# Performance work log

Hardware: AMD Instinct MI355X
Metric: run time of the kernel (lower is better)

Reference implementation:

```python
import jax, jax.numpy as jnp
import numpy as np

B, S, H = 64, 2048, 768
LAM = 0.0  # sparsegen-lin lambda (lam=0 -> sparsemax)
NEG = -1e30


def setup_inputs() -> dict:
    key = jax.random.key(0)
    k1, k2, k3, k4, k5 = jax.random.split(key, 5)
    hidden = jax.random.normal(k1, (B, S, H), jnp.float32)
    # contiguous entity spans of random length (>=16 valid tokens per example)
    lengths = jax.random.randint(k2, (B,), 16, S)
    mask1d = (jnp.arange(S)[None, :] < lengths[:, None]).astype(jnp.float32)
    token_mask = jnp.broadcast_to(mask1d[:, :, None], (B, S, H))
    pooled_tokens = jax.random.normal(k3, (B, H), jnp.float32)
    w_align = jax.random.normal(k4, (2 * H,), jnp.float32) * 0.02
    b_align = jax.random.normal(k5, (1,), jnp.float32) * 0.02
    return {"hidden": hidden, "token_mask": token_mask,
            "pooled_tokens": pooled_tokens, "w_align": w_align, "b_align": b_align}


def sparsegen_masked(scores, valid, lam):
    """Batched sparsegen-lin over valid positions only.
    scores: [B, S] float, valid: [B, S] bool. Returns probs [B, S] (0 at invalid).
    Matches per-example torch SparsegenLin applied to masked_select'd scores.
    """
    n = scores.shape[-1]
    zmax = jnp.max(jnp.where(valid, scores, -jnp.inf), axis=-1, keepdims=True)
    z = scores - zmax                                # subtract max over valid
    z_sortable = jnp.where(valid, z, NEG)
    zs = -jnp.sort(-z_sortable, axis=-1)             # descending; valid first
    n_valid = jnp.sum(valid, axis=-1, keepdims=True)
    ks = jnp.arange(1, n + 1, dtype=scores.dtype)[None, :]
    sorted_valid = ks <= n_valid.astype(scores.dtype)
    zs_m = jnp.where(sorted_valid, zs, 0.0)
    csum = jnp.cumsum(zs_m, axis=-1)
    bound = 1.0 - lam + ks * zs_m
    is_gt = (bound > csum) & sorted_valid
    k = jnp.maximum(jnp.max(jnp.where(is_gt, ks, 0.0), axis=-1, keepdims=True), 1.0)
    tau = (jnp.sum(jnp.where(is_gt, zs_m, 0.0), axis=-1, keepdims=True) - 1.0 + lam) / k
    ps = jnp.maximum((z - tau) / (1.0 - lam), 0.0)
    return jnp.where(valid, ps, 0.0)


def reference(hidden, token_mask, pooled_tokens, w_align, b_align):
    masked_hidden = hidden * token_mask                       # [B,S,H]
    tokens_rep_masked = pooled_tokens[:, None, :] * token_mask  # [B,S,H]
    # alignment_model(cat(tokens_rep_masked, masked_hidden)) -> [B,S]
    scores = (jnp.einsum('bsh,h->bs', tokens_rep_masked, w_align[:H])
              + jnp.einsum('bsh,h->bs', masked_hidden, w_align[H:])
              + b_align[0])
    attn_mask = token_mask[:, :, 0] > 0                       # [B,S] bool
    attention_probs = sparsegen_masked(scores, attn_mask, LAM)[:, :, None]  # [B,S,1]
    pooled = jnp.sum(masked_hidden * attention_probs, axis=1)  # [B,H]
    # insize == outsize -> output_layer is skipped (projected = pooled)
    return pooled, attention_probs
```

## Files before the change

kernel.cpp:

```cpp
#include <hip/hip_runtime.h>
#include <hip/hip_bf16.h>
#include <cstdint>
#include <cstddef>

#define BB 64
#define SS 2048
#define HH 768
#define LAM 0.0f
#define NEGV -1e30f

__global__ void scores_kernel(const float* __restrict__ hidden,
                              const float* __restrict__ token_mask,
                              const float* __restrict__ w_align,
                              float* __restrict__ scores) {
    int row = blockIdx.x * 4 + (threadIdx.x >> 6);
    int lane = threadIdx.x & 63;
    float m = token_mask[(size_t)row * HH];
    if (m == 0.0f) {
        if (lane == 0) scores[row] = NEGV;
        return;
    }
    const float* hrow = hidden + (size_t)row * HH;
    const float* w2 = w_align + HH;
    float acc = 0.f;
#pragma unroll
    for (int r = 0; r < 3; ++r) {
        int idx = r * 256 + lane * 4;
        float4 h = *reinterpret_cast<const float4*>(hrow + idx);
        float4 w = *reinterpret_cast<const float4*>(w2 + idx);
        acc += h.x * w.x + h.y * w.y + h.z * w.z + h.w * w.w;
    }
#pragma unroll
    for (int off = 32; off >= 1; off >>= 1) acc += __shfl_xor(acc, off);
    if (lane == 0) scores[row] = acc;
}

__device__ inline float breduce_sum(float v, float* red, int t) {
#pragma unroll
    for (int off = 32; off >= 1; off >>= 1) v += __shfl_xor(v, off);
    if ((t & 63) == 0) red[t >> 6] = v;
    __syncthreads();
    if (t < 16) {
        float x = red[t];
#pragma unroll
        for (int off = 8; off >= 1; off >>= 1) x += __shfl_xor(x, off);
        if (t == 0) red[0] = x;
    }
    __syncthreads();
    float r = red[0];
    __syncthreads();
    return r;
}

__device__ inline float breduce_max(float v, float* red, int t) {
#pragma unroll
    for (int off = 32; off >= 1; off >>= 1) v = fmaxf(v, __shfl_xor(v, off));
    if ((t & 63) == 0) red[t >> 6] = v;
    __syncthreads();
    if (t < 16) {
        float x = red[t];
#pragma unroll
        for (int off = 8; off >= 1; off >>= 1) x = fmaxf(x, __shfl_xor(x, off));
        if (t == 0) red[0] = x;
    }
    __syncthreads();
    float r = red[0];
    __syncthreads();
    return r;
}

__device__ inline float2 breduce_sum2(float a, float c, float2* red2, int t) {
#pragma unroll
    for (int off = 32; off >= 1; off >>= 1) {
        a += __shfl_xor(a, off);
        c += __shfl_xor(c, off);
    }
    if ((t & 63) == 0) red2[t >> 6] = make_float2(a, c);
    __syncthreads();
    if (t < 16) {
        float2 x = red2[t];
#pragma unroll
        for (int off = 8; off >= 1; off >>= 1) {
            x.x += __shfl_xor(x.x, off);
            x.y += __shfl_xor(x.y, off);
        }
        if (t == 0) red2[0] = x;
    }
    __syncthreads();
    float2 r = red2[0];
    __syncthreads();
    return r;
}

__global__ __launch_bounds__(1024, 1) void sparsemax_pool_kernel(
        const float* __restrict__ hidden,
        const float* __restrict__ pooled_tokens,
        const float* __restrict__ w_align,
        const float* __restrict__ b_align,
        const float* __restrict__ scores,
        float* __restrict__ out) {
    __shared__ float pl[SS];
    __shared__ int   sidx[SS];
    __shared__ float spv[SS];
    __shared__ float red[32];
    __shared__ float2 red2[16];
    __shared__ int   icnt;

    const int b = blockIdx.x;
    const int t = threadIdx.x;
    const int i0 = t, i1 = t + 1024;

    float v = (t < HH) ? pooled_tokens[b * HH + t] * w_align[t] : 0.f;
    float dotP = breduce_sum(v, red, t) + b_align[0];

    float r0 = scores[b * SS + i0];
    float r1 = scores[b * SS + i1];
    bool valid0 = r0 > -1e29f;
    bool valid1 = r1 > -1e29f;
    float s0 = r0 + dotP;
    float s1 = r1 + dotP;

    float mx = fmaxf(valid0 ? s0 : -INFINITY, valid1 ? s1 : -INFINITY);
    float zmax = breduce_max(mx, red, t);

    float z0 = valid0 ? (s0 - zmax) : NEGV;
    float z1 = valid1 ? (s1 - zmax) : NEGV;

    float tau = -1.0f;
#pragma unroll 1
    for (int it = 0; it < 50; ++it) {
        float a = (z0 > tau ? z0 : 0.f) + (z1 > tau ? z1 : 0.f);
        float c = (z0 > tau ? 1.f : 0.f) + (z1 > tau ? 1.f : 0.f);
        float2 sc = breduce_sum2(a, c, red2, t);
        float tn = (sc.x - 1.f + LAM) / sc.y;
        if (tn == tau) break;
        tau = tn;
    }

    const float inv = 1.f / (1.f - LAM);
    float p0 = valid0 ? fmaxf((z0 - tau) * inv, 0.f) : 0.f;
    float p1 = valid1 ? fmaxf((z1 - tau) * inv, 0.f) : 0.f;
    pl[i0] = p0;
    pl[i1] = p1;
    out[BB * HH + b * SS + i0] = p0;
    out[BB * HH + b * SS + i1] = p1;
    __syncthreads();

    if (t < 64) {
        int cnt = 0;
        for (int base = 0; base < SS; base += 64) {
            float p = pl[base + t];
            unsigned long long bal = __ballot(p > 0.f);
            if (p > 0.f) {
                int pos = cnt + (int)__popcll(bal & ((1ull << t) - 1ull));
                sidx[pos] = base + t;
                spv[pos] = p;
            }
            cnt += (int)__popcll(bal);
        }
        if (t == 0) icnt = cnt;
    }
    __syncthreads();
    int cnt = icnt;

    if (t < HH) {
        float acc = 0.f;
        for (int j = 0; j < cnt; ++j) {
            acc += spv[j] * hidden[(size_t)(b * SS + sidx[j]) * HH + t];
        }
        out[b * HH + t] = acc;
    }
}

extern "C" void kernel_launch(void* const* d_in, const int* in_sizes, int n_in,
                              void* d_out, int out_size, void* d_ws, size_t ws_size,
                              hipStream_t stream) {
    const float* hidden        = (const float*)d_in[0];
    const float* token_mask    = (const float*)d_in[1];
    const float* pooled_tokens = (const float*)d_in[2];
    const float* b_align       = (const float*)d_in[4];
    const float* w_align       = (const float*)d_in[3];
    float* out = (float*)d_out;

    float* scores_ws;
    if (ws_size >= (size_t)BB * SS * sizeof(float)) {
        scores_ws = (float*)d_ws;
    } else {
        scores_ws = out + BB * HH;
    }

    scores_kernel<<<dim3((BB * SS) / 4), dim3(256), 0, stream>>>(
        hidden, token_mask, w_align, scores_ws);

    sparsemax_pool_kernel<<<dim3(BB), dim3(1024), 0, stream>>>(
        hidden, pooled_tokens, w_align, b_align, scores_ws, out);
}
```

Baseline: 51.25 us.

## Assign one wavefront per batch row for sparsemax threshold and pooling

```diff
diff --git a/kernel.cpp b/kernel.cpp
--- a/kernel.cpp
+++ b/kernel.cpp
@@ -35,141 +35,104 @@
     if (lane == 0) scores[row] = acc;
 }
 
-__device__ inline float breduce_sum(float v, float* red, int t) {
-#pragma unroll
-    for (int off = 32; off >= 1; off >>= 1) v += __shfl_xor(v, off);
-    if ((t & 63) == 0) red[t >> 6] = v;
-    __syncthreads();
-    if (t < 16) {
-        float x = red[t];
-#pragma unroll
-        for (int off = 8; off >= 1; off >>= 1) x += __shfl_xor(x, off);
-        if (t == 0) red[0] = x;
-    }
-    __syncthreads();
-    float r = red[0];
-    __syncthreads();
-    return r;
-}
-
-__device__ inline float breduce_max(float v, float* red, int t) {
-#pragma unroll
-    for (int off = 32; off >= 1; off >>= 1) v = fmaxf(v, __shfl_xor(v, off));
-    if ((t & 63) == 0) red[t >> 6] = v;
-    __syncthreads();
-    if (t < 16) {
-        float x = red[t];
-#pragma unroll
-        for (int off = 8; off >= 1; off >>= 1) x = fmaxf(x, __shfl_xor(x, off));
-        if (t == 0) red[0] = x;
-    }
-    __syncthreads();
-    float r = red[0];
-    __syncthreads();
-    return r;
-}
-
-__device__ inline float2 breduce_sum2(float a, float c, float2* red2, int t) {
-#pragma unroll
-    for (int off = 32; off >= 1; off >>= 1) {
-        a += __shfl_xor(a, off);
-        c += __shfl_xor(c, off);
-    }
-    if ((t & 63) == 0) red2[t >> 6] = make_float2(a, c);
-    __syncthreads();
-    if (t < 16) {
-        float2 x = red2[t];
-#pragma unroll
-        for (int off = 8; off >= 1; off >>= 1) {
-            x.x += __shfl_xor(x.x, off);
-            x.y += __shfl_xor(x.y, off);
-        }
-        if (t == 0) red2[0] = x;
-    }
-    __syncthreads();
-    float2 r = red2[0];
-    __syncthreads();
-    return r;
-}
-
-__global__ __launch_bounds__(1024, 1) void sparsemax_pool_kernel(
+__global__ __launch_bounds__(256, 1) void tau_pool_kernel(
         const float* __restrict__ hidden,
         const float* __restrict__ pooled_tokens,
         const float* __restrict__ w_align,
         const float* __restrict__ b_align,
         const float* __restrict__ scores,
         float* __restrict__ out) {
-    __shared__ float pl[SS];
-    __shared__ int   sidx[SS];
-    __shared__ float spv[SS];
-    __shared__ float red[32];
-    __shared__ float2 red2[16];
-    __shared__ int   icnt;
+    const int b = (blockIdx.x * 256 + threadIdx.x) >> 6;
+    const int lane = threadIdx.x & 63;
 
-    const int b = blockIdx.x;
-    const int t = threadIdx.x;
-    const int i0 = t, i1 = t + 1024;
+    const float* pt = pooled_tokens + b * HH;
+    float dp = 0.f;
+#pragma unroll
+    for (int i = 0; i < 3; ++i) {
+        int idx = i * 256 + lane * 4;
+        float4 a = *reinterpret_cast<const float4*>(pt + idx);
+        float4 w = *reinterpret_cast<const float4*>(w_align + idx);
+        dp += a.x * w.x + a.y * w.y + a.z * w.z + a.w * w.w;
+    }
+#pragma unroll
+    for (int off = 32; off >= 1; off >>= 1) dp += __shfl_xor(dp, off);
+    dp += b_align[0];
 
-    float v = (t < HH) ? pooled_tokens[b * HH + t] * w_align[t] : 0.f;
-    float dotP = breduce_sum(v, red, t) + b_align[0];
+    const float* sc = scores + b * SS;
+    float z[32];
+#pragma unroll
+    for (int i = 0; i < 8; ++i) {
+        float4 v = *reinterpret_cast<const float4*>(sc + i * 256 + lane * 4);
+        z[i * 4 + 0] = v.x + dp;
+        z[i * 4 + 1] = v.y + dp;
+        z[i * 4 + 2] = v.z + dp;
+        z[i * 4 + 3] = v.w + dp;
+    }
 
-    float r0 = scores[b * SS + i0];
-    float r1 = scores[b * SS + i1];
-    bool valid0 = r0 > -1e29f;
-    bool valid1 = r1 > -1e29f;
-    float s0 = r0 + dotP;
-    float s1 = r1 + dotP;
-
-    float mx = fmaxf(valid0 ? s0 : -INFINITY, valid1 ? s1 : -INFINITY);
-    float zmax = breduce_max(mx, red, t);
-
-    float z0 = valid0 ? (s0 - zmax) : NEGV;
-    float z1 = valid1 ? (s1 - zmax) : NEGV;
+    float mx = z[0];
+#pragma unroll
+    for (int i = 1; i < 32; ++i) mx = fmaxf(mx, z[i]);
+#pragma unroll
+    for (int off = 32; off >= 1; off >>= 1) mx = fmaxf(mx, __shfl_xor(mx, off));
+#pragma unroll
+    for (int i = 0; i < 32; ++i) z[i] -= mx;
 
     float tau = -1.0f;
 #pragma unroll 1
     for (int it = 0; it < 50; ++it) {
-        float a = (z0 > tau ? z0 : 0.f) + (z1 > tau ? z1 : 0.f);
-        float c = (z0 > tau ? 1.f : 0.f) + (z1 > tau ? 1.f : 0.f);
-        float2 sc = breduce_sum2(a, c, red2, t);
-        float tn = (sc.x - 1.f + LAM) / sc.y;
+        float a = 0.f, c = 0.f;
+#pragma unroll
+        for (int i = 0; i < 32; ++i) {
+            bool g = z[i] > tau;
+            a += g ? z[i] : 0.f;
+            c += g ? 1.f : 0.f;
+        }
+#pragma unroll
+        for (int off = 32; off >= 1; off >>= 1) {
+            a += __shfl_xor(a, off);
+            c += __shfl_xor(c, off);
+        }
+        float tn = (a - 1.f + LAM) / c;
         if (tn == tau) break;
         tau = tn;
     }
 
     const float inv = 1.f / (1.f - LAM);
-    float p0 = valid0 ? fmaxf((z0 - tau) * inv, 0.f) : 0.f;
-    float p1 = valid1 ? fmaxf((z1 - tau) * inv, 0.f) : 0.f;
-    pl[i0] = p0;
-    pl[i1] = p1;
-    out[BB * HH + b * SS + i0] = p0;
-    out[BB * HH + b * SS + i1] = p1;
-    __syncthreads();
+    float p[32];
+#pragma unroll
+    for (int i = 0; i < 32; ++i) p[i] = fmaxf((z[i] - tau) * inv, 0.f);
+    float* po = out + BB * HH + b * SS;
+#pragma unroll
+    for (int i = 0; i < 8; ++i) {
+        float4 v = make_float4(p[i * 4 + 0], p[i * 4 + 1], p[i * 4 + 2], p[i * 4 + 3]);
+        *reinterpret_cast<float4*>(po + i * 256 + lane * 4) = v;
+    }
 
-    if (t < 64) {
-        int cnt = 0;
-        for (int base = 0; base < SS; base += 64) {
-            float p = pl[base + t];
-            unsigned long long bal = __ballot(p > 0.f);
-            if (p > 0.f) {
-                int pos = cnt + (int)__popcll(bal & ((1ull << t) - 1ull));
-                sidx[pos] = base + t;
-                spv[pos] = p;
+    float acc[12];
+#pragma unroll
+    for (int j = 0; j < 12; ++j) acc[j] = 0.f;
+    const float* hb = hidden + (size_t)b * SS * HH;
+#pragma unroll 1
+    for (int i = 0; i < 8; ++i) {
+#pragma unroll 1
+        for (int c = 0; c < 4; ++c) {
+            float pv = p[i * 4 + c];
+            unsigned long long m = __ballot(pv > 0.f);
+            while (m) {
+                int src = __ffsll((long long)m) - 1;
+                m &= m - 1;
+                float pb = __shfl(pv, src);
+                int sidx = i * 256 + src * 4 + c;
+                const float* hrow = hb + (size_t)sidx * HH;
+#pragma unroll
+                for (int j = 0; j < 12; ++j)
+                    acc[j] += pb * hrow[j * 64 + lane];
             }
-            cnt += (int)__popcll(bal);
         }
-        if (t == 0) icnt = cnt;
     }
-    __syncthreads();
-    int cnt = icnt;
-
-    if (t < HH) {
-        float acc = 0.f;
-        for (int j = 0; j < cnt; ++j) {
-            acc += spv[j] * hidden[(size_t)(b * SS + sidx[j]) * HH + t];
-        }
-        out[b * HH + t] = acc;
-    }
+#pragma unroll
+    for (int j = 0; j < 12; ++j)
+        out[b * HH + j * 64 + lane] = acc[j];
 }
 
 extern "C" void kernel_launch(void* const* d_in, const int* in_sizes, int n_in,
@@ -178,8 +141,8 @@
     const float* hidden        = (const float*)d_in[0];
     const float* token_mask    = (const float*)d_in[1];
     const float* pooled_tokens = (const float*)d_in[2];
+    const float* w_align       = (const float*)d_in[3];
     const float* b_align       = (const float*)d_in[4];
-    const float* w_align       = (const float*)d_in[3];
     float* out = (float*)d_out;
 
     float* scores_ws;
@@ -192,6 +155,6 @@
     scores_kernel<<<dim3((BB * SS) / 4), dim3(256), 0, stream>>>(
         hidden, token_mask, w_align, scores_ws);
 
-    sparsemax_pool_kernel<<<dim3(BB), dim3(1024), 0, stream>>>(
+    tau_pool_kernel<<<dim3(16), dim3(256), 0, stream>>>(
         hidden, pooled_tokens, w_align, b_align, scores_ws, out);
 }
```

Result: faster. 49.37 us (-3.7%).
